# Optimization experiments

Hardware: AMD Instinct MI355X
Metric: run time of the kernel (lower is better)

Reference implementation:

```python
import jax, jax.numpy as jnp
import numpy as np

INV_SQRT2 = 0.7071067811865476  # Haar (db1) filter coefficient


def haar_dwt(x):
    """Single-level Haar DWT along last axis (even length). Matches pywt db1."""
    e = x[..., 0::2]
    o = x[..., 1::2]
    ca = (e + o) * INV_SQRT2
    cd = (e - o) * INV_SQRT2
    return ca, cd


def haar_idwt(ca, cd):
    """Single-level Haar inverse DWT along last axis. Matches pywt waverec."""
    e = (ca + cd) * INV_SQRT2
    o = (ca - cd) * INV_SQRT2
    # interleave: out[2k]=e[k], out[2k+1]=o[k]
    return jnp.stack([e, o], axis=-1).reshape(ca.shape[:-1] + (2 * ca.shape[-1],))


def _soft_threshold(c, thr):
    a = jnp.abs(c)
    return jnp.where(a >= thr, jnp.sign(c) * (a - thr), jnp.zeros_like(c))


def setup_inputs() -> dict:
    key = jax.random.key(0)
    x = jax.random.normal(key, (64, 1024, 1024), dtype=jnp.float32)
    return {"x": x}


def reference(x):
    # x: [B, C, L]; 3-level Haar decomposition per (b, c) signal, vectorized.
    L = x.shape[-1]
    ca1, cd1 = haar_dwt(x)    # [B,C,L/2]
    ca2, cd2 = haar_dwt(ca1)  # [B,C,L/4]
    ca3, cd3 = haar_dwt(ca2)  # [B,C,L/8]

    # Universal threshold per signal: sigma = median(|cd1|)/0.6745,
    # lamda = sigma * sqrt(2*ln(L))  (natural log, as in math.log(L, e)).
    median_cd1 = jnp.median(jnp.abs(cd1), axis=-1, keepdims=True)  # [B,C,1]
    sigma = median_cd1 / 0.6745
    lamda = sigma * np.sqrt(2.0 * np.log(float(L))).astype(np.float32)

    # Per-level soft thresholds: lamda/log2(2), lamda/log2(3), lamda/log2(4).
    cd1 = _soft_threshold(cd1, lamda / np.float32(np.log2(2.0)))
    cd2 = _soft_threshold(cd2, lamda / np.float32(np.log2(3.0)))
    cd3 = _soft_threshold(cd3, lamda / np.float32(np.log2(4.0)))

    # Reconstruct with kept ca3 and thresholded details.
    ca2r = haar_idwt(ca3, cd3)
    ca1r = haar_idwt(ca2r, cd2)
    return haar_idwt(ca1r, cd1)
```

## Files before the change

### kernel.cpp

```cpp
#include <hip/hip_runtime.h>

#define L 1024
#define BLOCK 256

__device__ __forceinline__ float soft_thr(float c, float thr) {
    float a = fabsf(c);
    return (a >= thr) ? copysignf(a - thr, c) : 0.0f;
}

__global__ __launch_bounds__(BLOCK) void wavelet_denoise_kernel(
        const float* __restrict__ x, float* __restrict__ out) {
    constexpr float IS2 = 0.70710678118654752f;
    constexpr float SQRT_2LOGL = 3.7232974111f;

    const int lane = threadIdx.x & 63;
    const int wid  = threadIdx.x >> 6;
    const long long row = (long long)blockIdx.x * 4 + wid;
    const float* xr = x + row * L;
    float* orow = out + row * L;

    float4 in[4];
    #pragma unroll
    for (int j = 0; j < 4; ++j)
        in[j] = ((const float4*)xr)[j * 64 + lane];

    float ca1[8], cd1[8];
    #pragma unroll
    for (int j = 0; j < 4; ++j) {
        ca1[2*j]   = (in[j].x + in[j].y) * IS2;
        cd1[2*j]   = (in[j].x - in[j].y) * IS2;
        ca1[2*j+1] = (in[j].z + in[j].w) * IS2;
        cd1[2*j+1] = (in[j].z - in[j].w) * IS2;
    }

    float ca2[4], cd2[4];
    #pragma unroll
    for (int j = 0; j < 4; ++j) {
        ca2[j] = (ca1[2*j] + ca1[2*j+1]) * IS2;
        cd2[j] = (ca1[2*j] - ca1[2*j+1]) * IS2;
    }

    float ca3[4], cd3[4];
    #pragma unroll
    for (int j = 0; j < 4; ++j) {
        float o = __shfl_xor(ca2[j], 1);
        ca3[j] = (ca2[j] + o) * IS2;
        cd3[j] = (ca2[j] - o) * IS2;
    }

    float v[8];
    #pragma unroll
    for (int r = 0; r < 8; ++r) v[r] = fabsf(cd1[r]);

    const int i0 = lane << 3;
    #pragma unroll
    for (int k = 2; k <= 512; k <<= 1) {
        #pragma unroll
        for (int j = k >> 1; j > 0; j >>= 1) {
            if (j >= 8) {
                const int lmask = j >> 3;
                const bool keep_min = (((i0 & k) == 0) == ((lane & lmask) == 0));
                #pragma unroll
                for (int r = 0; r < 8; ++r) {
                    float o = __shfl_xor(v[r], lmask);
                    v[r] = keep_min ? fminf(v[r], o) : fmaxf(v[r], o);
                }
            } else {
                #pragma unroll
                for (int r = 0; r < 8; ++r) {
                    if ((r & j) == 0) {
                        const int p = r | j;
                        const bool up = (((i0 | r) & k) == 0);
                        float lo = fminf(v[r], v[p]);
                        float hi = fmaxf(v[r], v[p]);
                        v[r] = up ? lo : hi;
                        v[p] = up ? hi : lo;
                    }
                }
            }
        }
    }

    const float m0 = __shfl(v[7], 31);
    const float m1 = __shfl(v[0], 32);
    const float median = 0.5f * (m0 + m1);
    const float lam  = (median / 0.6745f) * SQRT_2LOGL;
    const float thr1 = lam;
    const float thr2 = lam / 1.5849625007f;
    const float thr3 = lam * 0.5f;

    #pragma unroll
    for (int j = 0; j < 4; ++j) {
        float c3 = __shfl(ca3[j], lane & 62);
        float d3 = soft_thr(__shfl(cd3[j], lane & 62), thr3);
        float ca2r = ((lane & 1) == 0) ? (c3 + d3) * IS2 : (c3 - d3) * IS2;

        float d2 = soft_thr(cd2[j], thr2);
        float ca1r0 = (ca2r + d2) * IS2;
        float ca1r1 = (ca2r - d2) * IS2;

        float d10 = soft_thr(cd1[2*j],   thr1);
        float d11 = soft_thr(cd1[2*j+1], thr1);
        float4 o;
        o.x = (ca1r0 + d10) * IS2;
        o.y = (ca1r0 - d10) * IS2;
        o.z = (ca1r1 + d11) * IS2;
        o.w = (ca1r1 - d11) * IS2;
        ((float4*)orow)[j * 64 + lane] = o;
    }
}

extern "C" void kernel_launch(void* const* d_in, const int* in_sizes, int n_in,
                              void* d_out, int out_size, void* d_ws, size_t ws_size,
                              hipStream_t stream) {
    const float* x = (const float*)d_in[0];
    float* out = (float*)d_out;
    const int rows = in_sizes[0] / L;
    wavelet_denoise_kernel<<<rows / 4, BLOCK, 0, stream>>>(x, out);
}
```

Baseline: 442.2 us.

## Replace float bitonic median sort with integer XOR-trick bitonic merge and partial final stage

Changes the median computation to work on the integer bit patterns of |cd1|, which preserve ordering for non-negative floats. Direction flips are done by XOR-ing with all-ones masks instead of per-pair conditional selects, and each lane begins with an 8-element in-lane sorting network. The final merge stage is shortened to a cross-lane exchange followed by a max/min reduction that extracts only the two middle elements. This is meant to cut ALU and select work in the compute-heavy sort, but the XOR bookkeeping is subtle and an error there would give a wrong median.

```diff
diff --git a/kernel.cpp b/kernel.cpp
--- a/kernel.cpp
+++ b/kernel.cpp
@@ -7,6 +7,9 @@
     float a = fabsf(c);
     return (a >= thr) ? copysignf(a - thr, c) : 0.0f;
 }
+
+__device__ __forceinline__ int imin2(int a, int b) { return (a < b) ? a : b; }
+__device__ __forceinline__ int imax2(int a, int b) { return (a > b) ? a : b; }
 
 __global__ __launch_bounds__(BLOCK) void wavelet_denoise_kernel(
         const float* __restrict__ x, float* __restrict__ out) {
@@ -48,41 +51,64 @@
         cd3[j] = (ca2[j] - o) * IS2;
     }
 
-    float v[8];
+    int w[8];
+    const int b0 = -(int)( lane       & 1);
+    const int b1 = -(int)((lane >> 1) & 1);
+    const int b2 = -(int)((lane >> 2) & 1);
+    const int b3 = -(int)((lane >> 3) & 1);
+    const int b4 = -(int)((lane >> 4) & 1);
+    const int b5 = -(int)((lane >> 5) & 1);
+
     #pragma unroll
-    for (int r = 0; r < 8; ++r) v[r] = fabsf(cd1[r]);
+    for (int r = 0; r < 8; ++r)
+        w[r] = (__float_as_int(cd1[r]) & 0x7fffffff) ^ b0;
 
-    const int i0 = lane << 3;
+    #define CE(a, c) { int _lo = imin2(w[a], w[c]); int _hi = imax2(w[a], w[c]); \
+                       w[a] = _lo; w[c] = _hi; }
+
+    CE(0,1) CE(2,3) CE(4,5) CE(6,7)
+    CE(0,2) CE(1,3) CE(4,6) CE(5,7)
+    CE(1,2) CE(5,6)
+    CE(0,4) CE(1,5) CE(2,6) CE(3,7)
+    CE(2,4) CE(3,5)
+    CE(1,2) CE(3,4) CE(5,6)
+
+    #define XORW(T) { const int _t = (T); \
+        _Pragma("unroll") for (int r = 0; r < 8; ++r) w[r] ^= _t; }
+
+    #define CROSS_STAGE(LM) { const bool _up = (lane & (LM)) != 0; \
+        _Pragma("unroll") for (int r = 0; r < 8; ++r) { \
+            int _o = __shfl_xor(w[r], (LM)); \
+            w[r] = _up ? imax2(w[r], _o) : imin2(w[r], _o); } }
+
+    #define INLANE3() { \
+        CE(0,4) CE(1,5) CE(2,6) CE(3,7) \
+        CE(0,2) CE(1,3) CE(4,6) CE(5,7) \
+        CE(0,1) CE(2,3) CE(4,5) CE(6,7) }
+
+    XORW(b0 ^ b1); CROSS_STAGE(1);                                                             INLANE3();
+    XORW(b1 ^ b2); CROSS_STAGE(2);  CROSS_STAGE(1);                                            INLANE3();
+    XORW(b2 ^ b3); CROSS_STAGE(4);  CROSS_STAGE(2); CROSS_STAGE(1);                            INLANE3();
+    XORW(b3 ^ b4); CROSS_STAGE(8);  CROSS_STAGE(4); CROSS_STAGE(2); CROSS_STAGE(1);            INLANE3();
+    XORW(b4 ^ b5); CROSS_STAGE(16); CROSS_STAGE(8); CROSS_STAGE(4); CROSS_STAGE(2); CROSS_STAGE(1); INLANE3();
+    XORW(b5);      CROSS_STAGE(32);
+
+    int zmx = imax2(imax2(imax2(w[0], w[1]), imax2(w[2], w[3])),
+                    imax2(imax2(w[4], w[5]), imax2(w[6], w[7])));
+    int zmn = imin2(imin2(imin2(w[0], w[1]), imin2(w[2], w[3])),
+                    imin2(imin2(w[4], w[5]), imin2(w[6], w[7])));
+    int z = (lane & 32) ? ~zmn : zmx;
     #pragma unroll
-    for (int k = 2; k <= 512; k <<= 1) {
-        #pragma unroll
-        for (int j = k >> 1; j > 0; j >>= 1) {
-            if (j >= 8) {
-                const int lmask = j >> 3;
-                const bool keep_min = (((i0 & k) == 0) == ((lane & lmask) == 0));
-                #pragma unroll
-                for (int r = 0; r < 8; ++r) {
-                    float o = __shfl_xor(v[r], lmask);
-                    v[r] = keep_min ? fminf(v[r], o) : fmaxf(v[r], o);
-                }
-            } else {
-                #pragma unroll
-                for (int r = 0; r < 8; ++r) {
-                    if ((r & j) == 0) {
-                        const int p = r | j;
-                        const bool up = (((i0 | r) & k) == 0);
-                        float lo = fminf(v[r], v[p]);
-                        float hi = fmaxf(v[r], v[p]);
-                        v[r] = up ? lo : hi;
-                        v[p] = up ? hi : lo;
-                    }
-                }
-            }
-        }
-    }
+    for (int m = 1; m <= 16; m <<= 1)
+        z = imax2(z, __shfl_xor(z, m));
+    const float m0 = __int_as_float(__shfl(z, 0));
+    const float m1 = __int_as_float(~__shfl(z, 32));
 
-    const float m0 = __shfl(v[7], 31);
-    const float m1 = __shfl(v[0], 32);
+    #undef CE
+    #undef XORW
+    #undef CROSS_STAGE
+    #undef INLANE3
+
     const float median = 0.5f * (m0 + m1);
     const float lam  = (median / 0.6745f) * SQRT_2LOGL;
     const float thr1 = lam;
```

Result: no change. 437.2 us (-1.1%).
